# Optimization experiments

Hardware: AMD Instinct MI355X
Metric: run time of the kernel (lower is better)

The kernel has to match this reference:

```python
import jax, jax.numpy as jnp
import numpy as np

B, R, U, D = 16, 2048, 2048, 1024
EPS_ATT = 1e-8
EPS_LN = 1e-6


def setup_inputs() -> dict:
    key = jax.random.key(0)
    ks = jax.random.split(key, 6)
    s = 1.0 / np.sqrt(D)
    return {
        "Q": jax.random.normal(ks[0], (B, R, D), dtype=jnp.float32),
        "K": jax.random.normal(ks[1], (B, U, D), dtype=jnp.float32),
        "V": jax.random.normal(ks[2], (B, U, D), dtype=jnp.float32),
        "W1": jax.random.normal(ks[3], (D, D), dtype=jnp.float32) * s,
        "b1": jnp.zeros((D,), dtype=jnp.float32),
        "W2": jax.random.normal(ks[4], (D, D), dtype=jnp.float32) * s,
        "b2": jnp.zeros((D,), dtype=jnp.float32),
        "gamma": jnp.ones((D,), dtype=jnp.float32),
        "beta": jnp.zeros((D,), dtype=jnp.float32),
    }


def reference(Q, K, V, W1, b1, W2, b2, gamma, beta):
    d_model = Q.shape[-1]
    # Faithful to source: sqrt(d_model + epsilon)
    scale = jnp.sqrt(jnp.asarray(d_model, jnp.float32) + EPS_ATT)
    scores = jnp.einsum('brd,bud->bru', Q, K) / scale  # [B,R,U]
    att = jax.nn.softmax(scores, axis=-1)
    V_att = jnp.einsum('bru,bud->brd', att, V)  # [B,R,D]

    def layer_norm(x):
        mu = jnp.mean(x, axis=-1, keepdims=True)
        var = jnp.mean(jnp.square(x - mu), axis=-1, keepdims=True)
        return gamma * (x - mu) / jnp.sqrt(var + EPS_LN) + beta

    X = layer_norm(Q + V_att)
    ffn = jnp.maximum(X @ W1 + b1, 0.0) @ W2 + b2
    return layer_norm(ffn + X)
```

## Files before the change

### kernel.cpp

```cpp
#include <hip/hip_runtime.h>
#include <math.h>
#include <stdint.h>

#define BATCH 16
#define RDIM 2048
#define UDIM 2048
#define DDIM 1024

typedef __attribute__((ext_vector_type(8))) short short8;
typedef __attribute__((ext_vector_type(4))) float f32x4;
typedef __attribute__((ext_vector_type(8))) unsigned short ushort8;
typedef __attribute__((ext_vector_type(4))) unsigned short ushort4v;
typedef __attribute__((ext_vector_type(4))) float float4v;

__device__ __forceinline__ float bf2f(unsigned short u) {
  unsigned int x = ((unsigned int)u) << 16;
  return __builtin_bit_cast(float, x);
}
__device__ __forceinline__ unsigned short f2bf(float f) {
  unsigned int x = __builtin_bit_cast(unsigned int, f);
  unsigned int r = (x + 0x7fffu + ((x >> 16) & 1u)) >> 16;
  return (unsigned short)r;
}

__device__ __forceinline__ void gload_lds16(const void* g, void* l) {
  __builtin_amdgcn_global_load_lds(
      (const __attribute__((address_space(1))) void*)(uintptr_t)g,
      (__attribute__((address_space(3))) void*)(uint32_t)(uintptr_t)l,
      16, 0, 0);
}

#define FENCE() __builtin_amdgcn_sched_barrier(0)
#define BAR() __builtin_amdgcn_s_barrier()
#define LGKM0() asm volatile("s_waitcnt lgkmcnt(0)" ::: "memory")
#define VMCNT8() asm volatile("s_waitcnt vmcnt(8)" ::: "memory")


__global__ __launch_bounds__(256) void k_conv_bf16(const float* __restrict__ in,
                                                   unsigned short* __restrict__ out,
                                                   float scale) {
  const long i = ((long)blockIdx.x * 256 + threadIdx.x) * 8;
  float4v a = *(const float4v*)(in + i);
  float4v b = *(const float4v*)(in + i + 4);
  ushort8 o;
#pragma unroll
  for (int j = 0; j < 4; ++j) o[j] = f2bf(a[j] * scale);
#pragma unroll
  for (int j = 0; j < 4; ++j) o[4 + j] = f2bf(b[j] * scale);
  *(ushort8*)(out + i) = o;
}

__global__ void k_transpose_bf16(const float* __restrict__ in,
                                 unsigned short* __restrict__ out,
                                 int rows, int cols, long sIn, long sOut) {
  __shared__ unsigned short tile[64][65];
  const long bz = blockIdx.z;
  in += bz * sIn;
  out += bz * sOut;
  const int r0 = blockIdx.x * 64;
  const int c0 = blockIdx.y * 64;
  const int tx = threadIdx.x;
  const int ty = threadIdx.y;
#pragma unroll
  for (int i = 0; i < 16; ++i) {
    const int r = ty + i * 4;
    tile[r][tx] = f2bf(in[(long)(r0 + r) * cols + c0 + tx]);
  }
  __syncthreads();
#pragma unroll
  for (int i = 0; i < 16; ++i) {
    const int r = ty + i * 4;
    out[(long)(c0 + r) * rows + r0 + tx] = tile[tx][r];
  }
}


template <int EPI>
__global__ __launch_bounds__(512, 2) void gemm_bt(
    const unsigned short* __restrict__ A, const unsigned short* __restrict__ B,
    void* __restrict__ Cout, int N, int K, long sA, long sB, long sC,
    const float* __restrict__ bias, const unsigned short* __restrict__ res) {
  __shared__ __align__(128) unsigned short lds[2][2][2][256 * 32];

  int lin = blockIdx.x + gridDim.x * (blockIdx.y + gridDim.y * blockIdx.z);
  lin = (lin & 7) * ((gridDim.x * gridDim.y * gridDim.z) >> 3) + (lin >> 3);
  const int by = lin % gridDim.y;
  int rest = lin / gridDim.y;
  const int bx = rest % gridDim.x;
  const int bz = rest / gridDim.x;

  const unsigned short* Ab = A + (long)bz * sA;
  const unsigned short* Bb = B + (long)bz * sB;

  const int tid = threadIdx.x;
  const int w = tid >> 6;
  const int lane = tid & 63;
  const int wm = w >> 2;
  const int wn = w & 3;
  const long rowBase = (long)bx * 256;
  const long colBase = (long)by * 256;

  const int stRow = w * 16 + (lane >> 2);
  const int stKc = ((lane & 3) ^ ((lane >> 3) & 3)) << 3;
  const unsigned short* gA = Ab + (rowBase + stRow) * (long)K + stKc;
  const unsigned short* gB = Bb + (colBase + stRow) * (long)K + stKc;
  const long qStep = (long)128 * K;
  char* ldsB = (char*)&lds[0][0][0][0];
  const int dOff = w * 1024;

  auto STAGE = [&](int buf, int op, int ks, int kadd) {
    const unsigned short* g = (op == 0 ? gA : gB) + kadd;
    char* d = ldsB + ((buf * 4 + op * 2 + ks) << 14) + dOff;
    gload_lds16(g, d);
    gload_lds16(g + qStep, d + 8192);
  };

  const int laneM = lane & 15;
  const int laneQ = lane >> 4;
  const int swz = (laneQ ^ ((laneM >> 1) & 3)) << 4;
  const int rdA = (wm * 128 + laneM) * 64 + swz;
  const int rdB = (wn * 64 + laneM) * 64 + swz;

  f32x4 acc[8][4] = {};
  const int NT = K >> 6;
  const int NTm1 = NT - 1;

  STAGE(0, 0, 0, 0);
  STAGE(0, 1, 0, 0);
  STAGE(0, 0, 1, 32);
  STAGE(0, 1, 1, 32);
  STAGE(1, 0, 0, 64);
  STAGE(1, 1, 0, 64);
  VMCNT8();
  BAR();
  FENCE();

  for (int t = 0; t < NT; ++t) {
    const int cur = t & 1;
    const int sA0 = (cur * 4 + 0) << 14;
    const int sA1 = (cur * 4 + 1) << 14;
    const int sB0 = (cur * 4 + 2) << 14;
    const int sB1 = (cur * 4 + 3) << 14;
    const int t1 = (t + 1 <= NTm1 ? t + 1 : NTm1);
    const int t2 = (t + 2 <= NTm1 ? t + 2 : NTm1);
    const int k1add = t1 * 64 + 32;
    const int k0add = t2 * 64;

    short8 a0[4], a1[4], b0[4];

#pragma unroll
    for (int m = 0; m < 4; ++m)
      a0[m] = *(const short8*)(ldsB + sA0 + rdA + m * 1024);
#pragma unroll
    for (int n = 0; n < 4; ++n)
      b0[n] = *(const short8*)(ldsB + sB0 + rdB + n * 1024);
    STAGE(cur ^ 1, 0, 1, k1add);
    FENCE();
    BAR();
    LGKM0();
    FENCE();
    __builtin_amdgcn_s_setprio(1);
#pragma unroll
    for (int m = 0; m < 4; ++m)
#pragma unroll
      for (int n = 0; n < 4; ++n)
        acc[m][n] = __builtin_amdgcn_mfma_f32_16x16x32_bf16(a0[m], b0[n],
                                                            acc[m][n], 0, 0, 0);
    __builtin_amdgcn_s_setprio(0);
    BAR();

#pragma unroll
    for (int m = 0; m < 4; ++m)
      a1[m] = *(const short8*)(ldsB + sA0 + rdA + (4 + m) * 1024);
    STAGE(cur ^ 1, 1, 1, k1add);
    FENCE();
    BAR();
    VMCNT8();
    LGKM0();
    FENCE();
    __builtin_amdgcn_s_setprio(1);
#pragma unroll
    for (int m = 0; m < 4; ++m)
#pragma unroll
      for (int n = 0; n < 4; ++n)
        acc[4 + m][n] = __builtin_amdgcn_mfma_f32_16x16x32_bf16(a1[m], b0[n],
                                                                acc[4 + m][n], 0, 0, 0);
    __builtin_amdgcn_s_setprio(0);
    BAR();

#pragma unroll
    for (int m = 0; m < 4; ++m)
      a0[m] = *(const short8*)(ldsB + sA1 + rdA + m * 1024);
#pragma unroll
    for (int n = 0; n < 4; ++n)
      b0[n] = *(const short8*)(ldsB + sB1 + rdB + n * 1024);
    STAGE(cur, 0, 0, k0add);
    FENCE();
    BAR();
    LGKM0();
    FENCE();
    __builtin_amdgcn_s_setprio(1);
#pragma unroll
    for (int m = 0; m < 4; ++m)
#pragma unroll
      for (int n = 0; n < 4; ++n)
        acc[m][n] = __builtin_amdgcn_mfma_f32_16x16x32_bf16(a0[m], b0[n],
                                                            acc[m][n], 0, 0, 0);
    __builtin_amdgcn_s_setprio(0);
    BAR();

#pragma unroll
    for (int m = 0; m < 4; ++m)
      a1[m] = *(const short8*)(ldsB + sA1 + rdA + (4 + m) * 1024);
    STAGE(cur, 1, 0, k0add);
    FENCE();
    BAR();
    VMCNT8();
    LGKM0();
    FENCE();
    __builtin_amdgcn_s_setprio(1);
#pragma unroll
    for (int m = 0; m < 4; ++m)
#pragma unroll
      for (int n = 0; n < 4; ++n)
        acc[4 + m][n] = __builtin_amdgcn_mfma_f32_16x16x32_bf16(a1[m], b0[n],
                                                                acc[4 + m][n], 0, 0, 0);
    __builtin_amdgcn_s_setprio(0);
    BAR();
  }

  const long r0 = rowBase + wm * 128;
  const long c0 = colBase + wn * 64;
  const int cr = (lane >> 4) << 2;
  const int cc = lane & 15;

  if constexpr (EPI == 0) {
    unsigned short* C = (unsigned short*)Cout + (long)bz * sC;
#pragma unroll
    for (int i = 0; i < 8; ++i)
#pragma unroll
      for (int j = 0; j < 4; ++j)
#pragma unroll
        for (int jj = 0; jj < 4; ++jj)
          C[(r0 + i * 16 + cr + jj) * N + (c0 + j * 16 + cc)] = f2bf(acc[i][j][jj]);
  } else if constexpr (EPI == 1) {
    unsigned short* C = (unsigned short*)Cout;
#pragma unroll
    for (int i = 0; i < 8; ++i)
#pragma unroll
      for (int j = 0; j < 4; ++j)
#pragma unroll
        for (int jj = 0; jj < 4; ++jj) {
          const long col = c0 + j * 16 + cc;
          float v = acc[i][j][jj] + bias[col];
          v = fmaxf(v, 0.f);
          C[(r0 + i * 16 + cr + jj) * N + col] = f2bf(v);
        }
  } else {
    float* C = (float*)Cout;
#pragma unroll
    for (int i = 0; i < 8; ++i)
#pragma unroll
      for (int j = 0; j < 4; ++j)
#pragma unroll
        for (int jj = 0; jj < 4; ++jj) {
          const long row = r0 + i * 16 + cr + jj;
          const long col = c0 + j * 16 + cc;
          C[row * N + col] = acc[i][j][jj] + bias[col] + bf2f(res[row * N + col]);
        }
  }
}


__global__ __launch_bounds__(256) void k_softmax(unsigned short* __restrict__ S) {
  __shared__ float red[8];
  const long base = (long)blockIdx.x * UDIM;
  const int t = threadIdx.x;
  ushort8 raw = *(const ushort8*)(S + base + t * 8);
  float v[8];
  float mx = -3.0e38f;
#pragma unroll
  for (int j = 0; j < 8; ++j) {
    v[j] = bf2f(raw[j]);
    mx = fmaxf(mx, v[j]);
  }
#pragma unroll
  for (int m = 32; m >= 1; m >>= 1) mx = fmaxf(mx, __shfl_xor(mx, m));
  const int wv = t >> 6;
  if ((t & 63) == 0) red[wv] = mx;
  __syncthreads();
  mx = fmaxf(fmaxf(red[0], red[1]), fmaxf(red[2], red[3]));
  float s = 0.f;
#pragma unroll
  for (int j = 0; j < 8; ++j) {
    v[j] = __expf(v[j] - mx);
    s += v[j];
  }
#pragma unroll
  for (int m = 32; m >= 1; m >>= 1) s += __shfl_xor(s, m);
  if ((t & 63) == 0) red[4 + wv] = s;
  __syncthreads();
  s = red[4] + red[5] + red[6] + red[7];
  const float rs = 1.f / s;
  ushort8 o;
#pragma unroll
  for (int j = 0; j < 8; ++j) o[j] = f2bf(v[j] * rs);
  *(ushort8*)(S + base + t * 8) = o;
}


__global__ __launch_bounds__(256) void k_addln_bf16(
    const float* __restrict__ Q, const unsigned short* __restrict__ Va,
    unsigned short* __restrict__ X, const float* __restrict__ gamma,
    const float* __restrict__ beta) {
  __shared__ float red[8];
  const long base = (long)blockIdx.x * DDIM;
  const int t = threadIdx.x;
  float4v q = *(const float4v*)(Q + base + t * 4);
  ushort4v a = *(const ushort4v*)(Va + base + t * 4);
  float x[4];
  float s = 0.f, ss = 0.f;
#pragma unroll
  for (int j = 0; j < 4; ++j) {
    x[j] = q[j] + bf2f(a[j]);
    s += x[j];
    ss += x[j] * x[j];
  }
#pragma unroll
  for (int m = 32; m >= 1; m >>= 1) {
    s += __shfl_xor(s, m);
    ss += __shfl_xor(ss, m);
  }
  const int wv = t >> 6;
  if ((t & 63) == 0) {
    red[wv] = s;
    red[4 + wv] = ss;
  }
  __syncthreads();
  s = red[0] + red[1] + red[2] + red[3];
  ss = red[4] + red[5] + red[6] + red[7];
  const float mu = s * (1.f / DDIM);
  const float var = ss * (1.f / DDIM) - mu * mu;
  const float rstd = rsqrtf(var + 1e-6f);
  ushort4v o;
#pragma unroll
  for (int j = 0; j < 4; ++j) {
    const int c = t * 4 + j;
    o[j] = f2bf(gamma[c] * ((x[j] - mu) * rstd) + beta[c]);
  }
  *(ushort4v*)(X + base + t * 4) = o;
}


__global__ __launch_bounds__(256) void k_ln_inplace(float* __restrict__ Y,
                                                    const float* __restrict__ gamma,
                                                    const float* __restrict__ beta) {
  __shared__ float red[8];
  const long base = (long)blockIdx.x * DDIM;
  const int t = threadIdx.x;
  float4v y = *(const float4v*)(Y + base + t * 4);
  float s = 0.f, ss = 0.f;
#pragma unroll
  for (int j = 0; j < 4; ++j) {
    s += y[j];
    ss += y[j] * y[j];
  }
#pragma unroll
  for (int m = 32; m >= 1; m >>= 1) {
    s += __shfl_xor(s, m);
    ss += __shfl_xor(ss, m);
  }
  const int wv = t >> 6;
  if ((t & 63) == 0) {
    red[wv] = s;
    red[4 + wv] = ss;
  }
  __syncthreads();
  s = red[0] + red[1] + red[2] + red[3];
  ss = red[4] + red[5] + red[6] + red[7];
  const float mu = s * (1.f / DDIM);
  const float var = ss * (1.f / DDIM) - mu * mu;
  const float rstd = rsqrtf(var + 1e-6f);
  float4v o;
#pragma unroll
  for (int j = 0; j < 4; ++j) {
    const int c = t * 4 + j;
    o[j] = gamma[c] * ((y[j] - mu) * rstd) + beta[c];
  }
  *(float4v*)(Y + base + t * 4) = o;
}


extern "C" void kernel_launch(void* const* d_in, const int* in_sizes, int n_in,
                              void* d_out, int out_size, void* d_ws, size_t ws_size,
                              hipStream_t stream) {
  const float* Q = (const float*)d_in[0];
  const float* Kin = (const float*)d_in[1];
  const float* V = (const float*)d_in[2];
  const float* W1 = (const float*)d_in[3];
  const float* b1 = (const float*)d_in[4];
  const float* W2 = (const float*)d_in[5];
  const float* b2 = (const float*)d_in[6];
  const float* gamma = (const float*)d_in[7];
  const float* beta = (const float*)d_in[8];
  float* out = (float*)d_out;

  const long nQ = (long)BATCH * RDIM * DDIM;
  const long nK = (long)BATCH * UDIM * DDIM;
  const long nS = (long)BATCH * RDIM * UDIM;

  char* w = (char*)d_ws;
  unsigned short* Qb = (unsigned short*)w;  w += nQ * 2;
  unsigned short* Kb = (unsigned short*)w;  w += nK * 2;
  unsigned short* Vt = (unsigned short*)w;  w += nK * 2;
  unsigned short* S  = (unsigned short*)w;  w += nS * 2;
  unsigned short* X  = (unsigned short*)w;  w += nQ * 2;
  unsigned short* W1t = (unsigned short*)w; w += (long)DDIM * DDIM * 2;
  unsigned short* W2t = (unsigned short*)w; w += (long)DDIM * DDIM * 2;
  unsigned short* Va = Qb;
  unsigned short* H  = S;

  const float scale = 1.0f / sqrtf(1024.0f + 1e-8f);

  k_conv_bf16<<<nQ / 2048, 256, 0, stream>>>(Q, Qb, scale);
  k_conv_bf16<<<nK / 2048, 256, 0, stream>>>(Kin, Kb, 1.0f);
  k_transpose_bf16<<<dim3(UDIM / 64, DDIM / 64, BATCH), dim3(64, 4), 0, stream>>>(
      V, Vt, UDIM, DDIM, (long)UDIM * DDIM, (long)UDIM * DDIM);
  k_transpose_bf16<<<dim3(DDIM / 64, DDIM / 64, 1), dim3(64, 4), 0, stream>>>(
      W1, W1t, DDIM, DDIM, 0, 0);
  k_transpose_bf16<<<dim3(DDIM / 64, DDIM / 64, 1), dim3(64, 4), 0, stream>>>(
      W2, W2t, DDIM, DDIM, 0, 0);

  gemm_bt<0><<<dim3(RDIM / 256, UDIM / 256, BATCH), 512, 0, stream>>>(
      Qb, Kb, S, UDIM, DDIM, (long)RDIM * DDIM, (long)UDIM * DDIM, (long)RDIM * UDIM,
      nullptr, nullptr);
  k_softmax<<<BATCH * RDIM, 256, 0, stream>>>(S);
  gemm_bt<0><<<dim3(RDIM / 256, DDIM / 256, BATCH), 512, 0, stream>>>(
      S, Vt, Va, DDIM, UDIM, (long)RDIM * UDIM, (long)DDIM * UDIM, (long)RDIM * DDIM,
      nullptr, nullptr);
  k_addln_bf16<<<BATCH * RDIM, 256, 0, stream>>>(Q, Va, X, gamma, beta);
  gemm_bt<1><<<dim3(BATCH * RDIM / 256, DDIM / 256, 1), 512, 0, stream>>>(
      X, W1t, H, DDIM, DDIM, 0, 0, 0, b1, nullptr);
  gemm_bt<2><<<dim3(BATCH * RDIM / 256, DDIM / 256, 1), 512, 0, stream>>>(
      H, W2t, out, DDIM, DDIM, 0, 0, 0, b2, X);
  k_ln_inplace<<<BATCH * RDIM, 256, 0, stream>>>(out, gamma, beta);
}
```

Measured before the change: 690.5 us.

## Restructure GEMM main loop to one barrier per K-tile with full prefetch

Reworks the bf16 GEMM main loop from four barrier-separated sub-phases, each staging a quarter tile, into a single-barrier-per-iteration schedule. All fragments of the current tile are read from LDS up front, the whole next tile is staged with global_load_lds, and partial lgkmcnt waits let MFMAs start while later LDS reads are still in flight. This cuts barrier and synchronisation overhead and raises register use for the extra fragments. The vmcnt(0) wait at the end of each iteration may expose global-load latency that the old two-tile lookahead was hiding.

```diff
diff --git a/kernel.cpp b/kernel.cpp
--- a/kernel.cpp
+++ b/kernel.cpp
@@ -33,7 +33,9 @@
 #define FENCE() __builtin_amdgcn_sched_barrier(0)
 #define BAR() __builtin_amdgcn_s_barrier()
 #define LGKM0() asm volatile("s_waitcnt lgkmcnt(0)" ::: "memory")
-#define VMCNT8() asm volatile("s_waitcnt vmcnt(8)" ::: "memory")
+#define LGKM4() asm volatile("s_waitcnt lgkmcnt(4)" ::: "memory")
+#define LGKM8() asm volatile("s_waitcnt lgkmcnt(8)" ::: "memory")
+#define VMCNT0() asm volatile("s_waitcnt vmcnt(0)" ::: "memory")
 
 
 __global__ __launch_bounds__(256) void k_conv_bf16(const float* __restrict__ in,
@@ -126,27 +128,24 @@
   const int NTm1 = NT - 1;
 
   STAGE(0, 0, 0, 0);
+  STAGE(0, 0, 1, 32);
   STAGE(0, 1, 0, 0);
-  STAGE(0, 0, 1, 32);
   STAGE(0, 1, 1, 32);
-  STAGE(1, 0, 0, 64);
-  STAGE(1, 1, 0, 64);
-  VMCNT8();
+  VMCNT0();
   BAR();
   FENCE();
 
   for (int t = 0; t < NT; ++t) {
     const int cur = t & 1;
+    const int nxt = cur ^ 1;
     const int sA0 = (cur * 4 + 0) << 14;
     const int sA1 = (cur * 4 + 1) << 14;
     const int sB0 = (cur * 4 + 2) << 14;
     const int sB1 = (cur * 4 + 3) << 14;
-    const int t1 = (t + 1 <= NTm1 ? t + 1 : NTm1);
-    const int t2 = (t + 2 <= NTm1 ? t + 2 : NTm1);
-    const int k1add = t1 * 64 + 32;
-    const int k0add = t2 * 64;
-
-    short8 a0[4], a1[4], b0[4];
+    const int tn = (t + 1 <= NTm1 ? t + 1 : NTm1);
+    const int ka = tn * 64;
+
+    short8 a0[4], a1[4], a2[4], a3[4], b0[4], b1[4];
 
 #pragma unroll
     for (int m = 0; m < 4; ++m)
@@ -154,10 +153,13 @@
 #pragma unroll
     for (int n = 0; n < 4; ++n)
       b0[n] = *(const short8*)(ldsB + sB0 + rdB + n * 1024);
-    STAGE(cur ^ 1, 0, 1, k1add);
-    FENCE();
-    BAR();
-    LGKM0();
+    FENCE();
+#pragma unroll
+    for (int m = 0; m < 4; ++m)
+      a1[m] = *(const short8*)(ldsB + sA0 + rdA + (4 + m) * 1024);
+    STAGE(nxt, 0, 0, ka);
+    STAGE(nxt, 0, 1, ka + 32);
+    LGKM4();
     FENCE();
     __builtin_amdgcn_s_setprio(1);
 #pragma unroll
@@ -167,16 +169,16 @@
         acc[m][n] = __builtin_amdgcn_mfma_f32_16x16x32_bf16(a0[m], b0[n],
                                                             acc[m][n], 0, 0, 0);
     __builtin_amdgcn_s_setprio(0);
-    BAR();
-
-#pragma unroll
-    for (int m = 0; m < 4; ++m)
-      a1[m] = *(const short8*)(ldsB + sA0 + rdA + (4 + m) * 1024);
-    STAGE(cur ^ 1, 1, 1, k1add);
-    FENCE();
-    BAR();
-    VMCNT8();
-    LGKM0();
+
+#pragma unroll
+    for (int m = 0; m < 4; ++m)
+      a2[m] = *(const short8*)(ldsB + sA1 + rdA + m * 1024);
+#pragma unroll
+    for (int n = 0; n < 4; ++n)
+      b1[n] = *(const short8*)(ldsB + sB1 + rdB + n * 1024);
+    STAGE(nxt, 1, 0, ka);
+    STAGE(nxt, 1, 1, ka + 32);
+    LGKM8();
     FENCE();
     __builtin_amdgcn_s_setprio(1);
 #pragma unroll
@@ -186,36 +188,21 @@
         acc[4 + m][n] = __builtin_amdgcn_mfma_f32_16x16x32_bf16(a1[m], b0[n],
                                                                 acc[4 + m][n], 0, 0, 0);
     __builtin_amdgcn_s_setprio(0);
-    BAR();
-
-#pragma unroll
-    for (int m = 0; m < 4; ++m)
-      a0[m] = *(const short8*)(ldsB + sA1 + rdA + m * 1024);
-#pragma unroll
-    for (int n = 0; n < 4; ++n)
-      b0[n] = *(const short8*)(ldsB + sB1 + rdB + n * 1024);
-    STAGE(cur, 0, 0, k0add);
-    FENCE();
-    BAR();
-    LGKM0();
+
+#pragma unroll
+    for (int m = 0; m < 4; ++m)
+      a3[m] = *(const short8*)(ldsB + sA1 + rdA + (4 + m) * 1024);
+    LGKM4();
     FENCE();
     __builtin_amdgcn_s_setprio(1);
 #pragma unroll
     for (int m = 0; m < 4; ++m)
 #pragma unroll
       for (int n = 0; n < 4; ++n)
-        acc[m][n] = __builtin_amdgcn_mfma_f32_16x16x32_bf16(a0[m], b0[n],
+        acc[m][n] = __builtin_amdgcn_mfma_f32_16x16x32_bf16(a2[m], b1[n],
                                                             acc[m][n], 0, 0, 0);
     __builtin_amdgcn_s_setprio(0);
-    BAR();
-
-#pragma unroll
-    for (int m = 0; m < 4; ++m)
-      a1[m] = *(const short8*)(ldsB + sA1 + rdA + (4 + m) * 1024);
-    STAGE(cur, 1, 0, k0add);
-    FENCE();
-    BAR();
-    VMCNT8();
+
     LGKM0();
     FENCE();
     __builtin_amdgcn_s_setprio(1);
@@ -223,10 +210,13 @@
     for (int m = 0; m < 4; ++m)
 #pragma unroll
       for (int n = 0; n < 4; ++n)
-        acc[4 + m][n] = __builtin_amdgcn_mfma_f32_16x16x32_bf16(a1[m], b0[n],
+        acc[4 + m][n] = __builtin_amdgcn_mfma_f32_16x16x32_bf16(a3[m], b1[n],
                                                                 acc[4 + m][n], 0, 0, 0);
     __builtin_amdgcn_s_setprio(0);
+    FENCE();
+    VMCNT0();
     BAR();
+    FENCE();
   }
 
   const long r0 = rowBase + wm * 128;
```

New measurement: 665.6 us. 1.04x faster.
